# Performance work log

Measured on AMD Instinct MI355X. Metric: run time of the kernel, lower is better.

The kernel has to match this reference:

```python
import jax, jax.numpy as jnp
import numpy as np
from functools import partial

N_USERS = 100000
N_ITEMS = 50000
EMB = 64
N_FACTORS = 4
N_ITER = 2
N_LAYERS = 2
E = 2000000
EPS = 1e-12  # F.normalize eps


def setup_inputs() -> dict:
    key = jax.random.key(0)
    k1, k2, k3, k4 = jax.random.split(key, 4)
    N = N_USERS + N_ITEMS
    user_emb = jax.random.normal(k1, (N_USERS, EMB), jnp.float32) * 0.1
    item_emb = jax.random.normal(k2, (N_ITEMS, EMB), jnp.float32) * 0.1
    # first N entries cover every node once so row/col degree sums are > 0
    # (original norm_adj has no isolated nodes; avoids 1/sqrt(0))
    h = jnp.concatenate([jnp.arange(N, dtype=jnp.int32),
                         jax.random.randint(k3, (E - N,), 0, N, jnp.int32)])
    t = jnp.concatenate([jnp.arange(N, dtype=jnp.int32)[::-1],
                         jax.random.randint(k4, (E - N,), 0, N, jnp.int32)])
    return {"user_emb": user_emb, "item_emb": item_emb, "h_list": h, "t_list": t}


def _l2norm(x):
    n = jnp.sqrt(jnp.sum(x * x, axis=-1, keepdims=True))
    return x / jnp.maximum(n, EPS)


def _dgcf_embed(user_emb, item_emb, h_list, t_list):
    N = user_emb.shape[0] + item_emb.shape[0]
    d = user_emb.shape[1]
    F = N_FACTORS
    df = d // F
    Ee = h_list.shape[0]
    seg = partial(jax.ops.segment_sum, num_segments=N)
    seg_h = jax.vmap(lambda v: seg(v, h_list))  # batched over factor axis

    ego = jnp.concatenate([user_emb, item_emb], 0)  # [N, d]
    all_embeds = [ego]
    A_values = jnp.ones((F, Ee), ego.dtype)  # routing logits, persist across layers

    for _ in range(N_LAYERS):
        x = ego.reshape(N, F, df).transpose(1, 0, 2)  # [F, N, df] factor chunks
        out = x
        for _ in range(N_ITER):
            scores = jax.nn.softmax(A_values, axis=0)        # [F, E]
            rowsum = seg_h(scores)                           # [F, N] sparse.sum(A, dim=1)
            d_col = 1.0 / jnp.sqrt(rowsum)                   # [F, N]
            # out = D_col @ A @ D_col @ x  (original uses D_col on both sides)
            y = d_col[:, :, None] * x                        # [F, N, df]
            msg = scores[:, :, None] * y[:, t_list, :]       # [F, E, df]
            out = d_col[:, :, None] * seg_h(msg)             # [F, N, df]
            # routing score update: cosine-ish affinity head(new) vs tanh(tail(old))
            head = _l2norm(out[:, h_list, :])                # [F, E, df]
            tail = _l2norm(x[:, t_list, :])                  # [F, E, df]
            A_values = A_values + jnp.sum(head * jnp.tanh(tail), axis=-1)
        ego = out.transpose(1, 0, 2).reshape(N, d)           # concat factor outputs
        all_embeds.append(ego)

    all_emb = jnp.mean(jnp.stack(all_embeds, 1), axis=1)     # [N, d]
    return all_emb[:user_emb.shape[0]], all_emb[user_emb.shape[0]:]


def reference(user_emb, item_emb, h_list, t_list):
    return _dgcf_embed(user_emb, item_emb, h_list, t_list)
```

## Files before the change

kernel.cpp:

```cpp
#include <hip/hip_runtime.h>
#include <hip/hip_bf16.h>

#define DEMB 64
typedef unsigned short u16;

__device__ __forceinline__ u16 f2bf(float f) {
    union { float f; unsigned int i; } c; c.f = f;
    unsigned int r = c.i + 0x7FFF + ((c.i >> 16) & 1);
    return (u16)(r >> 16);
}
__device__ __forceinline__ float lo16(unsigned int w) {
    union { unsigned int i; float f; } c; c.i = w << 16; return c.f;
}
__device__ __forceinline__ float hi16(unsigned int w) {
    union { unsigned int i; float f; } c; c.i = w & 0xFFFF0000u; return c.f;
}

__device__ __forceinline__ float ptanh5(float a) {
    float a2 = a * a;
    float t = fmaf(a2, -0.030095f, 0.124066f);
    t = fmaf(a2, t, -0.332377f);
    t = fmaf(a2, t, 1.0f);
    return a * t;
}

__global__ void init_A_kernel(float4* __restrict__ A, int E) {
    int e = blockIdx.x * blockDim.x + threadIdx.x;
    if (e < E) A[e] = make_float4(1.f, 1.f, 1.f, 1.f);
}

__global__ void concat_copy_kernel(const float* __restrict__ u, const float* __restrict__ it,
                                   float* __restrict__ x, float* __restrict__ acc,
                                   int nu_elems, int total) {
    int i = blockIdx.x * blockDim.x + threadIdx.x;
    if (i >= total) return;
    float v = (i < nu_elems) ? u[i] : it[i - nu_elems];
    x[i] = v;
    acc[i] = v;
}

__global__ void hist_kernel(const int* __restrict__ h, int* __restrict__ ghist,
                            int E, int EPB, int NB) {
    __shared__ int bins[1024];
    int b = blockIdx.x, tid = threadIdx.x;
    for (int j = tid; j < NB; j += 256) bins[j] = 0;
    __syncthreads();
    int s = b * EPB, e = min(s + EPB, E);
    for (int k = s + tid; k < e; k += 256)
        atomicAdd(&bins[((unsigned)h[k]) >> 8], 1);
    __syncthreads();
    for (int j = tid; j < NB; j += 256) ghist[j * gridDim.x + b] = bins[j];
}

__global__ void btot_kernel(const int* __restrict__ ghist, int* __restrict__ btot) {
    __shared__ int s[256];
    int j = blockIdx.x, tid = threadIdx.x;
    s[tid] = ghist[j * 256 + tid];
    __syncthreads();
    for (int o = 128; o >= 1; o >>= 1) {
        if (tid < o) s[tid] += s[tid + o];
        __syncthreads();
    }
    if (tid == 0) btot[j] = s[0];
}

__global__ void bscan_kernel(const int* __restrict__ btot, int* __restrict__ bbase,
                             int NB, int E) {
    __shared__ int s[1024];
    int tid = threadIdx.x;
    int v = (tid < NB) ? btot[tid] : 0;
    s[tid] = v;
    __syncthreads();
    for (int o = 1; o < 1024; o <<= 1) {
        int a = (tid >= o) ? s[tid - o] : 0;
        __syncthreads();
        s[tid] += a;
        __syncthreads();
    }
    if (tid < NB) bbase[tid] = s[tid] - v;
    if (tid == 0) bbase[NB] = E;
}

__global__ void bofs_kernel(int* __restrict__ ghist, const int* __restrict__ bbase) {
    __shared__ int s[256];
    int j = blockIdx.x, tid = threadIdx.x;
    int v = ghist[j * 256 + tid];
    s[tid] = v;
    __syncthreads();
    for (int o = 1; o < 256; o <<= 1) {
        int a = (tid >= o) ? s[tid - o] : 0;
        __syncthreads();
        s[tid] += a;
        __syncthreads();
    }
    ghist[j * 256 + tid] = bbase[j] + s[tid] - v;
}

__global__ void scatter_kernel(const int* __restrict__ h, const int* __restrict__ t,
                               const int* __restrict__ ghist, unsigned* __restrict__ stg,
                               int E, int EPB, int NB) {
    __shared__ int cur[1024];
    int b = blockIdx.x, tid = threadIdx.x;
    for (int j = tid; j < NB; j += 256) cur[j] = ghist[j * gridDim.x + b];
    __syncthreads();
    int s = b * EPB, e = min(s + EPB, E);
    for (int k = s + tid; k < e; k += 256) {
        unsigned hh = (unsigned)h[k];
        int pos = atomicAdd(&cur[hh >> 8], 1);
        stg[pos] = ((hh & 255u) << 18) | (unsigned)t[k];
    }
}

__global__ void finalize_kernel(const unsigned* __restrict__ stg, const int* __restrict__ bbase,
                                int* __restrict__ off, int* __restrict__ csr_t, int N, int E) {
    __shared__ int cnt[256];
    __shared__ int scn[256];
    int b = blockIdx.x, tid = threadIdx.x;
    int ebeg = bbase[b], eend = bbase[b + 1];
    cnt[tid] = 0;
    __syncthreads();
    for (int k = ebeg + tid; k < eend; k += 256)
        atomicAdd(&cnt[(stg[k] >> 18) & 255u], 1);
    __syncthreads();
    int v = cnt[tid];
    scn[tid] = v;
    __syncthreads();
    for (int o = 1; o < 256; o <<= 1) {
        int a = (tid >= o) ? scn[tid - o] : 0;
        __syncthreads();
        scn[tid] += a;
        __syncthreads();
    }
    int excl = scn[tid] - v;
    int gn = (b << 8) + tid;
    if (gn < N) off[gn] = ebeg + excl;
    if (b == 0 && tid == 0) off[N] = E;
    __syncthreads();
    cnt[tid] = excl;
    __syncthreads();
    for (int k = ebeg + tid; k < eend; k += 256) {
        unsigned en = stg[k];
        int slot = atomicAdd(&cnt[(en >> 18) & 255u], 1);
        csr_t[ebeg + slot] = (int)(en & 0x3FFFFu);
    }
}

__global__ void dcol0_kernel(const int* __restrict__ off, float* __restrict__ dcol, int N) {
    int n = blockIdx.x * blockDim.x + threadIdx.x;
    if (n >= N) return;
    float v = 0.5f * rsqrtf((float)(off[n + 1] - off[n]));
    *(float4*)(dcol + (size_t)n * 4) = make_float4(v, v, v, v);
}

__global__ void prep_kernel(const float* __restrict__ x, u16* __restrict__ xs,
                            u16* __restrict__ tailt, int total) {
    int i = blockIdx.x * blockDim.x + threadIdx.x;
    if (i >= total) return;
    float v = x[i];
    xs[i] = f2bf(v);
    float s = v * v;
#pragma unroll
    for (int o = 8; o >= 1; o >>= 1) s += __shfl_xor(s, o);
    float nr = fmaxf(sqrtf(s), 1e-12f);
    tailt[i] = f2bf(ptanh5(v * __builtin_amdgcn_rcpf(nr)));
}

template <bool UNI, bool WOUT, bool ROUTE>
__global__ void message_kernel(const int* __restrict__ off, const int* __restrict__ csr_t,
                               float* __restrict__ Acsr, float* __restrict__ prob,
                               const u16* __restrict__ xs, const u16* __restrict__ tailt,
                               const float* __restrict__ dcol_in, float* __restrict__ dcol_out,
                               float* __restrict__ out, int N) {
    int gid = blockIdx.x * blockDim.x + threadIdx.x;
    int n = gid >> 6;
    if (n >= N) return;
    int l = gid & 63;
    int g = l >> 4;
    int m = l & 15;
    int f = m >> 2;
    int s = off[n], e = off[n + 1];

    float a0 = 0.f, a1 = 0.f, a2 = 0.f, a3 = 0.f;

#pragma unroll 2
    for (int k = s; k < e; k += 8) {
        int e1 = k + g, e2 = e1 + 4;
        bool v1 = e1 < e, v2 = e2 < e;
        int c1 = v1 ? e1 : s;
        int c2 = v2 ? e2 : s;
        int t1 = csr_t[c1], t2 = csr_t[c2];
        float p1, p2;
        if (UNI) {
            p1 = dcol_in[t1 * 4 + f];
            p2 = dcol_in[t2 * 4 + f];
        } else {
            p1 = prob[(size_t)c1 * 4 + f] * dcol_in[t1 * 4 + f];
            p2 = prob[(size_t)c2 * 4 + f] * dcol_in[t2 * 4 + f];
        }
        p1 = v1 ? p1 : 0.f;
        p2 = v2 ? p2 : 0.f;
        const uint2 x1 = *(const uint2*)(xs + ((size_t)t1 << 6) + (m << 2));
        const uint2 x2 = *(const uint2*)(xs + ((size_t)t2 << 6) + (m << 2));
        a0 += p1 * lo16(x1.x) + p2 * lo16(x2.x);
        a1 += p1 * hi16(x1.x) + p2 * hi16(x2.x);
        a2 += p1 * lo16(x1.y) + p2 * lo16(x2.y);
        a3 += p1 * hi16(x1.y) + p2 * hi16(x2.y);
    }

    a0 += __shfl_xor(a0, 16); a1 += __shfl_xor(a1, 16);
    a2 += __shfl_xor(a2, 16); a3 += __shfl_xor(a3, 16);
    a0 += __shfl_xor(a0, 32); a1 += __shfl_xor(a1, 32);
    a2 += __shfl_xor(a2, 32); a3 += __shfl_xor(a3, 32);

    if (WOUT) {
        float dn = dcol_in[n * 4 + f];
        if (l < 16) {
            *(float4*)(out + ((size_t)n << 6) + (m << 2)) =
                make_float4(a0 * dn, a1 * dn, a2 * dn, a3 * dn);
        }
    }
    if (!ROUTE) return;

    float ss = a0 * a0 + a1 * a1 + a2 * a2 + a3 * a3;
    ss += __shfl_xor(ss, 1);
    ss += __shfl_xor(ss, 2);
    float inv = 1.0f / fmaxf(sqrtf(ss), 1e-12f);
    float h0 = a0 * inv, h1 = a1 * inv, h2 = a2 * inv, h3 = a3 * inv;

    float rowsumf = 0.f;

#pragma unroll 2
    for (int k = s; k < e; k += 8) {
        int e1 = k + g, e2 = e1 + 4;
        bool v1 = e1 < e, v2 = e2 < e;
        int c1 = v1 ? e1 : s;
        int c2 = v2 ? e2 : s;
        int t1 = csr_t[c1], t2 = csr_t[c2];
        const uint2 tv1 = *(const uint2*)(tailt + ((size_t)t1 << 6) + (m << 2));
        const uint2 tv2 = *(const uint2*)(tailt + ((size_t)t2 << 6) + (m << 2));
        float d1 = h0 * lo16(tv1.x) + h1 * hi16(tv1.x)
                 + h2 * lo16(tv1.y) + h3 * hi16(tv1.y);
        float d2 = h0 * lo16(tv2.x) + h1 * hi16(tv2.x)
                 + h2 * lo16(tv2.y) + h3 * hi16(tv2.y);
        d1 += __shfl_xor(d1, 1); d1 += __shfl_xor(d1, 2);
        d2 += __shfl_xor(d2, 1); d2 += __shfl_xor(d2, 2);
        float na1 = Acsr[(size_t)c1 * 4 + f] + d1;
        float na2 = Acsr[(size_t)c2 * 4 + f] + d2;
        float ex1 = __expf(na1);
        float ex2 = __expf(na2);
        float se1 = ex1 + __shfl_xor(ex1, 4); se1 += __shfl_xor(se1, 8);
        float se2 = ex2 + __shfl_xor(ex2, 4); se2 += __shfl_xor(se2, 8);
        float p1 = ex1 * __builtin_amdgcn_rcpf(se1);
        float p2 = ex2 * __builtin_amdgcn_rcpf(se2);
        if ((m & 3) == 0) {
            if (v1) { Acsr[(size_t)e1 * 4 + f] = na1; prob[(size_t)e1 * 4 + f] = p1; }
            if (v2) { Acsr[(size_t)e2 * 4 + f] = na2; prob[(size_t)e2 * 4 + f] = p2; }
        }
        rowsumf += (v1 ? p1 : 0.f) + (v2 ? p2 : 0.f);
    }

    rowsumf += __shfl_xor(rowsumf, 16);
    rowsumf += __shfl_xor(rowsumf, 32);
    if (l < 16 && (m & 3) == 0) dcol_out[n * 4 + f] = rsqrtf(rowsumf);
}

__global__ void acc_kernel(float* __restrict__ acc, const float* __restrict__ v, int n, int final_) {
    int i = blockIdx.x * blockDim.x + threadIdx.x;
    if (i >= n) return;
    float r = acc[i] + v[i];
    acc[i] = final_ ? r * (1.0f / 3.0f) : r;
}

extern "C" void kernel_launch(void* const* d_in, const int* in_sizes, int n_in,
                              void* d_out, int out_size, void* d_ws, size_t ws_size,
                              hipStream_t stream) {
    const float* user_emb = (const float*)d_in[0];
    const float* item_emb = (const float*)d_in[1];
    const int* h = (const int*)d_in[2];
    const int* t = (const int*)d_in[3];

    const int nu_elems = in_sizes[0];
    const int ni_elems = in_sizes[1];
    const int total = nu_elems + ni_elems;
    const int N = total / DEMB;
    const int E = in_sizes[2];
    const int NB = (N + 255) >> 8;
    const int NBLK = 256;
    const int EPB = (E + NBLK - 1) / NBLK;

    float* acc = (float*)d_out;

    float* x     = (float*)d_ws;
    float* out   = x + (size_t)total;
    float* Acsr  = out + (size_t)total;
    float* prob  = Acsr + (size_t)4 * E;
    float* dcolA = prob + (size_t)4 * E;
    float* dcolB = dcolA + (size_t)4 * N;
    u16* xs      = (u16*)(dcolB + (size_t)4 * N);
    u16* tailt   = xs + (size_t)total;
    int* ghist   = (int*)(tailt + (size_t)total);
    int* btot    = ghist + (size_t)NB * 256;
    int* bbase   = btot + ((NB + 3) & ~3);
    int* off     = bbase + ((NB + 5) & ~3);
    int* csr_t   = off + ((N + 4) & ~3);
    unsigned* stg = (unsigned*)prob;

    const int BLK = 256;
    const int gE = (E + BLK - 1) / BLK;
    const int gTot = (total + BLK - 1) / BLK;
    const int gN = (N + BLK - 1) / BLK;
    const int gNodeWave = (N * 64 + BLK - 1) / BLK;

    concat_copy_kernel<<<gTot, BLK, 0, stream>>>(user_emb, item_emb, x, acc, nu_elems, total);

    hist_kernel<<<NBLK, 256, 0, stream>>>(h, ghist, E, EPB, NB);
    btot_kernel<<<NB, 256, 0, stream>>>(ghist, btot);
    bscan_kernel<<<1, 1024, 0, stream>>>(btot, bbase, NB, E);
    bofs_kernel<<<NB, 256, 0, stream>>>(ghist, bbase);
    scatter_kernel<<<NBLK, 256, 0, stream>>>(h, t, ghist, stg, E, EPB, NB);
    finalize_kernel<<<NB, 256, 0, stream>>>(stg, bbase, off, csr_t, N, E);

    init_A_kernel<<<gE, BLK, 0, stream>>>((float4*)Acsr, E);
    dcol0_kernel<<<gN, BLK, 0, stream>>>(off, dcolA, N);

    prep_kernel<<<gTot, BLK, 0, stream>>>(x, xs, tailt, total);
    message_kernel<true, false, true><<<gNodeWave, BLK, 0, stream>>>(
        off, csr_t, Acsr, prob, xs, tailt, dcolA, dcolB, out, N);
    message_kernel<false, true, true><<<gNodeWave, BLK, 0, stream>>>(
        off, csr_t, Acsr, prob, xs, tailt, dcolB, dcolA, out, N);
    acc_kernel<<<gTot, BLK, 0, stream>>>(acc, out, total, 0);

    prep_kernel<<<gTot, BLK, 0, stream>>>(out, xs, tailt, total);
    message_kernel<false, false, true><<<gNodeWave, BLK, 0, stream>>>(
        off, csr_t, Acsr, prob, xs, tailt, dcolA, dcolB, x, N);
    message_kernel<false, true, false><<<gNodeWave, BLK, 0, stream>>>(
        off, csr_t, Acsr, prob, xs, tailt, dcolB, dcolA, x, N);
    acc_kernel<<<gTot, BLK, 0, stream>>>(acc, x, total, 1);
}
```

Before: 608.1 us.

## Pad CSR rows to multiples of four with a zero sentinel node

Builds a padded CSR in which each node's neighbour list is rounded up to a multiple of four. The padding entries point at a sentinel node N whose embedding and dcol are zero. The message kernel can then drop the per-edge validity checks and clamped indices, and each lane group handles one edge per step instead of two. This needs an extra two-pass finalize and scan, plus extra buffers (deg, two offset arrays). Halving the edges per loop iteration lowers ILP and may raise the iteration count, and padded slots cost some wasted gathers.

```diff
diff --git a/kernel.cpp b/kernel.cpp
--- a/kernel.cpp
+++ b/kernel.cpp
@@ -64,11 +64,11 @@
     if (tid == 0) btot[j] = s[0];
 }
 
-__global__ void bscan_kernel(const int* __restrict__ btot, int* __restrict__ bbase,
-                             int NB, int E) {
+__global__ void bscan_kernel(const int* __restrict__ in, int* __restrict__ outp,
+                             int NB, int tail) {
     __shared__ int s[1024];
     int tid = threadIdx.x;
-    int v = (tid < NB) ? btot[tid] : 0;
+    int v = (tid < NB) ? in[tid] : 0;
     s[tid] = v;
     __syncthreads();
     for (int o = 1; o < 1024; o <<= 1) {
@@ -77,8 +77,8 @@
         s[tid] += a;
         __syncthreads();
     }
-    if (tid < NB) bbase[tid] = s[tid] - v;
-    if (tid == 0) bbase[NB] = E;
+    if (tid < NB) outp[tid] = s[tid] - v;
+    if (tid == 0) outp[NB] = tail;
 }
 
 __global__ void bofs_kernel(int* __restrict__ ghist, const int* __restrict__ bbase) {
@@ -111,10 +111,10 @@
     }
 }
 
-__global__ void finalize_kernel(const unsigned* __restrict__ stg, const int* __restrict__ bbase,
-                                int* __restrict__ off, int* __restrict__ csr_t, int N, int E) {
+__global__ void finalize_a_kernel(const unsigned* __restrict__ stg, const int* __restrict__ bbase,
+                                  int* __restrict__ deg, int* __restrict__ ptot, int N) {
     __shared__ int cnt[256];
-    __shared__ int scn[256];
+    __shared__ int red[256];
     int b = blockIdx.x, tid = threadIdx.x;
     int ebeg = bbase[b], eend = bbase[b + 1];
     cnt[tid] = 0;
@@ -122,41 +122,75 @@
     for (int k = ebeg + tid; k < eend; k += 256)
         atomicAdd(&cnt[(stg[k] >> 18) & 255u], 1);
     __syncthreads();
-    int v = cnt[tid];
-    scn[tid] = v;
+    int d = cnt[tid];
+    int gn = (b << 8) + tid;
+    if (gn < N) deg[gn] = d;
+    int pd = (d + 3) & ~3;
+    red[tid] = pd;
+    __syncthreads();
+    for (int o = 128; o >= 1; o >>= 1) {
+        if (tid < o) red[tid] += red[tid + o];
+        __syncthreads();
+    }
+    if (tid == 0) ptot[b] = red[0];
+}
+
+__global__ void finalize_b_kernel(const unsigned* __restrict__ stg, const int* __restrict__ bbase,
+                                  const int* __restrict__ pbase2, const int* __restrict__ deg,
+                                  int* __restrict__ off_pad, int* __restrict__ off_upad,
+                                  int* __restrict__ csr_t, int N) {
+    __shared__ int scn[256];
+    __shared__ int scn2[256];
+    __shared__ int cur[256];
+    int b = blockIdx.x, tid = threadIdx.x;
+    int ebeg = bbase[b], eend = bbase[b + 1];
+    int gn = (b << 8) + tid;
+    int d = (gn < N) ? deg[gn] : 0;
+    int pd = (d + 3) & ~3;
+    scn[tid] = pd;
+    scn2[tid] = d;
     __syncthreads();
     for (int o = 1; o < 256; o <<= 1) {
         int a = (tid >= o) ? scn[tid - o] : 0;
+        int a2 = (tid >= o) ? scn2[tid - o] : 0;
         __syncthreads();
         scn[tid] += a;
-        __syncthreads();
-    }
-    int excl = scn[tid] - v;
-    int gn = (b << 8) + tid;
-    if (gn < N) off[gn] = ebeg + excl;
-    if (b == 0 && tid == 0) off[N] = E;
-    __syncthreads();
-    cnt[tid] = excl;
+        scn2[tid] += a2;
+        __syncthreads();
+    }
+    int pexcl = scn[tid] - pd;
+    int uexcl = scn2[tid] - d;
+    int pb = pbase2[b];
+    int base = pb + pexcl;
+    if (gn < N) {
+        off_pad[gn] = base;
+        off_upad[gn] = ebeg + uexcl;
+    }
+    cur[tid] = pexcl;
     __syncthreads();
     for (int k = ebeg + tid; k < eend; k += 256) {
         unsigned en = stg[k];
-        int slot = atomicAdd(&cnt[(en >> 18) & 255u], 1);
-        csr_t[ebeg + slot] = (int)(en & 0x3FFFFu);
-    }
-}
-
-__global__ void dcol0_kernel(const int* __restrict__ off, float* __restrict__ dcol, int N) {
+        int slot = atomicAdd(&cur[(en >> 18) & 255u], 1);
+        csr_t[pb + slot] = (int)(en & 0x3FFFFu);
+    }
+    __syncthreads();
+    for (int q = d; q < pd; q++) csr_t[base + q] = N;
+}
+
+__global__ void dcol0_kernel(const int* __restrict__ deg, float* __restrict__ dcolA,
+                             float* __restrict__ dcolB, int N) {
     int n = blockIdx.x * blockDim.x + threadIdx.x;
-    if (n >= N) return;
-    float v = 0.5f * rsqrtf((float)(off[n + 1] - off[n]));
-    *(float4*)(dcol + (size_t)n * 4) = make_float4(v, v, v, v);
+    if (n > N) return;
+    float v = (n < N) ? 0.5f * rsqrtf((float)deg[n]) : 0.f;
+    *(float4*)(dcolA + (size_t)n * 4) = make_float4(v, v, v, v);
+    if (n == N) *(float4*)(dcolB + (size_t)n * 4) = make_float4(0.f, 0.f, 0.f, 0.f);
 }
 
 __global__ void prep_kernel(const float* __restrict__ x, u16* __restrict__ xs,
                             u16* __restrict__ tailt, int total) {
     int i = blockIdx.x * blockDim.x + threadIdx.x;
-    if (i >= total) return;
-    float v = x[i];
+    if (i >= total + DEMB) return;
+    float v = (i < total) ? x[i] : 0.f;
     xs[i] = f2bf(v);
     float s = v * v;
 #pragma unroll
@@ -166,7 +200,8 @@
 }
 
 template <bool UNI, bool WOUT, bool ROUTE>
-__global__ void message_kernel(const int* __restrict__ off, const int* __restrict__ csr_t,
+__global__ void message_kernel(const int* __restrict__ off_pad, const int* __restrict__ off_upad,
+                               const int* __restrict__ deg, const int* __restrict__ csr_t,
                                float* __restrict__ Acsr, float* __restrict__ prob,
                                const u16* __restrict__ xs, const u16* __restrict__ tailt,
                                const float* __restrict__ dcol_in, float* __restrict__ dcol_out,
@@ -178,33 +213,29 @@
     int g = l >> 4;
     int m = l & 15;
     int f = m >> 2;
-    int s = off[n], e = off[n + 1];
+    int s = off_pad[n];
+    int dg = deg[n];
+    int dp = (dg + 3) & ~3;
+    const int* ct = csr_t + s;
+    unsigned pbase = (unsigned)off_upad[n] * 4u + (unsigned)(g * 4 + f);
+    unsigned moff = (unsigned)(m << 2);
 
     float a0 = 0.f, a1 = 0.f, a2 = 0.f, a3 = 0.f;
 
 #pragma unroll 2
-    for (int k = s; k < e; k += 8) {
-        int e1 = k + g, e2 = e1 + 4;
-        bool v1 = e1 < e, v2 = e2 < e;
-        int c1 = v1 ? e1 : s;
-        int c2 = v2 ? e2 : s;
-        int t1 = csr_t[c1], t2 = csr_t[c2];
-        float p1, p2;
+    for (int kk = 0; kk < dp; kk += 4) {
+        unsigned t1 = (unsigned)ct[kk + g];
+        float p1;
         if (UNI) {
-            p1 = dcol_in[t1 * 4 + f];
-            p2 = dcol_in[t2 * 4 + f];
+            p1 = dcol_in[t1 * 4u + (unsigned)f];
         } else {
-            p1 = prob[(size_t)c1 * 4 + f] * dcol_in[t1 * 4 + f];
-            p2 = prob[(size_t)c2 * 4 + f] * dcol_in[t2 * 4 + f];
+            p1 = prob[pbase + (unsigned)kk * 4u] * dcol_in[t1 * 4u + (unsigned)f];
         }
-        p1 = v1 ? p1 : 0.f;
-        p2 = v2 ? p2 : 0.f;
-        const uint2 x1 = *(const uint2*)(xs + ((size_t)t1 << 6) + (m << 2));
-        const uint2 x2 = *(const uint2*)(xs + ((size_t)t2 << 6) + (m << 2));
-        a0 += p1 * lo16(x1.x) + p2 * lo16(x2.x);
-        a1 += p1 * hi16(x1.x) + p2 * hi16(x2.x);
-        a2 += p1 * lo16(x1.y) + p2 * lo16(x2.y);
-        a3 += p1 * hi16(x1.y) + p2 * hi16(x2.y);
+        const uint2 x1 = *(const uint2*)(xs + (t1 << 6) + moff);
+        a0 += p1 * lo16(x1.x);
+        a1 += p1 * hi16(x1.x);
+        a2 += p1 * lo16(x1.y);
+        a3 += p1 * hi16(x1.y);
     }
 
     a0 += __shfl_xor(a0, 16); a1 += __shfl_xor(a1, 16);
@@ -213,9 +244,9 @@
     a2 += __shfl_xor(a2, 32); a3 += __shfl_xor(a3, 32);
 
     if (WOUT) {
-        float dn = dcol_in[n * 4 + f];
+        float dn = dcol_in[(unsigned)n * 4u + (unsigned)f];
         if (l < 16) {
-            *(float4*)(out + ((size_t)n << 6) + (m << 2)) =
+            *(float4*)(out + ((unsigned)n << 6) + moff) =
                 make_float4(a0 * dn, a1 * dn, a2 * dn, a3 * dn);
         }
     }
@@ -230,38 +261,25 @@
     float rowsumf = 0.f;
 
 #pragma unroll 2
-    for (int k = s; k < e; k += 8) {
-        int e1 = k + g, e2 = e1 + 4;
-        bool v1 = e1 < e, v2 = e2 < e;
-        int c1 = v1 ? e1 : s;
-        int c2 = v2 ? e2 : s;
-        int t1 = csr_t[c1], t2 = csr_t[c2];
-        const uint2 tv1 = *(const uint2*)(tailt + ((size_t)t1 << 6) + (m << 2));
-        const uint2 tv2 = *(const uint2*)(tailt + ((size_t)t2 << 6) + (m << 2));
+    for (int kk = 0; kk < dp; kk += 4) {
+        unsigned t1 = (unsigned)ct[kk + g];
+        const uint2 tv1 = *(const uint2*)(tailt + (t1 << 6) + moff);
         float d1 = h0 * lo16(tv1.x) + h1 * hi16(tv1.x)
                  + h2 * lo16(tv1.y) + h3 * hi16(tv1.y);
-        float d2 = h0 * lo16(tv2.x) + h1 * hi16(tv2.x)
-                 + h2 * lo16(tv2.y) + h3 * hi16(tv2.y);
         d1 += __shfl_xor(d1, 1); d1 += __shfl_xor(d1, 2);
-        d2 += __shfl_xor(d2, 1); d2 += __shfl_xor(d2, 2);
-        float na1 = Acsr[(size_t)c1 * 4 + f] + d1;
-        float na2 = Acsr[(size_t)c2 * 4 + f] + d2;
+        unsigned ai = pbase + (unsigned)kk * 4u;
+        float na1 = Acsr[ai] + d1;
         float ex1 = __expf(na1);
-        float ex2 = __expf(na2);
         float se1 = ex1 + __shfl_xor(ex1, 4); se1 += __shfl_xor(se1, 8);
-        float se2 = ex2 + __shfl_xor(ex2, 4); se2 += __shfl_xor(se2, 8);
         float p1 = ex1 * __builtin_amdgcn_rcpf(se1);
-        float p2 = ex2 * __builtin_amdgcn_rcpf(se2);
-        if ((m & 3) == 0) {
-            if (v1) { Acsr[(size_t)e1 * 4 + f] = na1; prob[(size_t)e1 * 4 + f] = p1; }
-            if (v2) { Acsr[(size_t)e2 * 4 + f] = na2; prob[(size_t)e2 * 4 + f] = p2; }
-        }
-        rowsumf += (v1 ? p1 : 0.f) + (v2 ? p2 : 0.f);
+        bool v1 = (kk + g) < dg;
+        if ((m & 3) == 0 && v1) { Acsr[ai] = na1; prob[ai] = p1; }
+        rowsumf += v1 ? p1 : 0.f;
     }
 
     rowsumf += __shfl_xor(rowsumf, 16);
     rowsumf += __shfl_xor(rowsumf, 32);
-    if (l < 16 && (m & 3) == 0) dcol_out[n * 4 + f] = rsqrtf(rowsumf);
+    if (l < 16 && (m & 3) == 0) dcol_out[(unsigned)n * 4u + (unsigned)f] = rsqrtf(rowsumf);
 }
 
 __global__ void acc_kernel(float* __restrict__ acc, const float* __restrict__ v, int n, int final_) {
@@ -287,6 +305,7 @@
     const int NB = (N + 255) >> 8;
     const int NBLK = 256;
     const int EPB = (E + NBLK - 1) / NBLK;
+    const int EPAD = E + 3 * N + 256;
 
     float* acc = (float*)d_out;
 
@@ -295,20 +314,25 @@
     float* Acsr  = out + (size_t)total;
     float* prob  = Acsr + (size_t)4 * E;
     float* dcolA = prob + (size_t)4 * E;
-    float* dcolB = dcolA + (size_t)4 * N;
-    u16* xs      = (u16*)(dcolB + (size_t)4 * N);
-    u16* tailt   = xs + (size_t)total;
-    int* ghist   = (int*)(tailt + (size_t)total);
+    float* dcolB = dcolA + (size_t)4 * (N + 1);
+    u16* xs      = (u16*)(dcolB + (size_t)4 * (N + 1));
+    u16* tailt   = xs + (size_t)(total + DEMB);
+    int* ghist   = (int*)(tailt + (size_t)(total + DEMB));
     int* btot    = ghist + (size_t)NB * 256;
-    int* bbase   = btot + ((NB + 3) & ~3);
-    int* off     = bbase + ((NB + 5) & ~3);
-    int* csr_t   = off + ((N + 4) & ~3);
+    int* ptot    = btot + ((NB + 3) & ~3);
+    int* bbase   = ptot + ((NB + 3) & ~3);
+    int* pbase2  = bbase + ((NB + 5) & ~3);
+    int* deg     = pbase2 + ((NB + 5) & ~3);
+    int* off_pad = deg + ((N + 3) & ~3);
+    int* off_upad= off_pad + ((N + 3) & ~3);
+    int* csr_t   = off_upad + ((N + 3) & ~3);
     unsigned* stg = (unsigned*)prob;
 
     const int BLK = 256;
     const int gE = (E + BLK - 1) / BLK;
     const int gTot = (total + BLK - 1) / BLK;
-    const int gN = (N + BLK - 1) / BLK;
+    const int gTot2 = (total + DEMB + BLK - 1) / BLK;
+    const int gN1 = (N + 1 + BLK - 1) / BLK;
     const int gNodeWave = (N * 64 + BLK - 1) / BLK;
 
     concat_copy_kernel<<<gTot, BLK, 0, stream>>>(user_emb, item_emb, x, acc, nu_elems, total);
@@ -318,22 +342,25 @@
     bscan_kernel<<<1, 1024, 0, stream>>>(btot, bbase, NB, E);
     bofs_kernel<<<NB, 256, 0, stream>>>(ghist, bbase);
     scatter_kernel<<<NBLK, 256, 0, stream>>>(h, t, ghist, stg, E, EPB, NB);
-    finalize_kernel<<<NB, 256, 0, stream>>>(stg, bbase, off, csr_t, N, E);
+    finalize_a_kernel<<<NB, 256, 0, stream>>>(stg, bbase, deg, ptot, N);
+    bscan_kernel<<<1, 1024, 0, stream>>>(ptot, pbase2, NB, 0);
+    finalize_b_kernel<<<NB, 256, 0, stream>>>(stg, bbase, pbase2, deg, off_pad, off_upad,
+                                              csr_t, N);
 
     init_A_kernel<<<gE, BLK, 0, stream>>>((float4*)Acsr, E);
-    dcol0_kernel<<<gN, BLK, 0, stream>>>(off, dcolA, N);
-
-    prep_kernel<<<gTot, BLK, 0, stream>>>(x, xs, tailt, total);
+    dcol0_kernel<<<gN1, BLK, 0, stream>>>(deg, dcolA, dcolB, N);
+
+    prep_kernel<<<gTot2, BLK, 0, stream>>>(x, xs, tailt, total);
     message_kernel<true, false, true><<<gNodeWave, BLK, 0, stream>>>(
-        off, csr_t, Acsr, prob, xs, tailt, dcolA, dcolB, out, N);
+        off_pad, off_upad, deg, csr_t, Acsr, prob, xs, tailt, dcolA, dcolB, out, N);
     message_kernel<false, true, true><<<gNodeWave, BLK, 0, stream>>>(
-        off, csr_t, Acsr, prob, xs, tailt, dcolB, dcolA, out, N);
+        off_pad, off_upad, deg, csr_t, Acsr, prob, xs, tailt, dcolB, dcolA, out, N);
     acc_kernel<<<gTot, BLK, 0, stream>>>(acc, out, total, 0);
 
-    prep_kernel<<<gTot, BLK, 0, stream>>>(out, xs, tailt, total);
+    prep_kernel<<<gTot2, BLK, 0, stream>>>(out, xs, tailt, total);
     message_kernel<false, false, true><<<gNodeWave, BLK, 0, stream>>>(
-        off, csr_t, Acsr, prob, xs, tailt, dcolA, dcolB, x, N);
+        off_pad, off_upad, deg, csr_t, Acsr, prob, xs, tailt, dcolA, dcolB, x, N);
     message_kernel<false, true, false><<<gNodeWave, BLK, 0, stream>>>(
-        off, csr_t, Acsr, prob, xs, tailt, dcolB, dcolA, x, N);
+        off_pad, off_upad, deg, csr_t, Acsr, prob, xs, tailt, dcolB, dcolA, x, N);
     acc_kernel<<<gTot, BLK, 0, stream>>>(acc, x, total, 1);
 }
```

Result: slower. 828.0 us (+36.2%).
